# Optimization experiments

Hardware: AMD Instinct MI355X
Metric: run time of the kernel (lower is better)

The kernel has to match this reference:

```python
import jax, jax.numpy as jnp
import numpy as np

N = 65536   # batch_size * timeseries
D = 512     # feature dim of h_real
K = 64      # n_clusters


def setup_inputs() -> dict:
    key = jax.random.key(0)
    k1, k2 = jax.random.split(key)
    h_real = jax.random.normal(k1, (N, D), dtype=jnp.float32)
    # F is an (approximately) orthogonal projection parameter [N, K].
    F = jax.random.normal(k2, (N, K), dtype=jnp.float32)
    return {"h_real": h_real, "F": F}


def reference(h_real, F):
    # Original: WTW = h h^T (N x N); loss = trace(WTW) - trace(F^T WTW F).
    # Algebraically identical reduced form, never materializing the N x N Gram:
    #   trace(h h^T) = sum(h * h)
    #   trace(F^T h h^T F) = ||F^T h||_F^2
    tr_wtw = jnp.sum(h_real * h_real)
    G = F.T @ h_real                      # [K, D] skinny GEMM
    tr_proj = jnp.sum(G * G)
    return tr_wtw - tr_proj
```

## Files before the change

kernel.cpp:

```cpp
#include <hip/hip_runtime.h>
#include <hip/hip_fp16.h>

#define N_TOT 65536
#define D_DIM 512
#define K_DIM 64
#define NC    32
#define HT_S  40
#define GSZ   (K_DIM * D_DIM)

typedef __bf16   bf16x8 __attribute__((ext_vector_type(8)));
typedef float    f32x4  __attribute__((ext_vector_type(4)));
typedef float    f32x2  __attribute__((ext_vector_type(2)));
typedef _Float16 half8  __attribute__((ext_vector_type(8)));

__device__ __forceinline__ unsigned int pack_bf16(float a, float b) {
    union { float f; unsigned int u; } x, y;
    x.f = a; y.f = b;
    unsigned int lo = (x.u + 0x7fffu + ((x.u >> 16) & 1u)) >> 16;
    unsigned int hi = (y.u + 0x7fffu + ((y.u >> 16) & 1u)) >> 16;
    return lo | (hi << 16);
}

extern "C" __global__ void __launch_bounds__(1024)
k1_partial(const float* __restrict__ h, const float* __restrict__ F,
           float* __restrict__ trw_out, unsigned short* __restrict__ gpart,
           float* __restrict__ out, int rowsPerBlock) {
    __shared__ unsigned short ht[2][D_DIM * HT_S];
    __shared__ unsigned short Ft[2][K_DIM * HT_S];
    __shared__ float red[16];

    const int tid = threadIdx.x;
    const int b   = blockIdx.x;
    if (b == 0 && tid == 0) out[0] = 0.0f;

    const int row0    = b * rowsPerBlock;
    const int nChunks = rowsPerBlock / NC;

    const int sd = tid & 127;
    const int sg = tid >> 7;
    const int fk = (tid & 31) * 2;
    const int fg = tid >> 5;
    const int wave = tid >> 6;
    const int lane = tid & 63;
    const int m    = lane & 15;
    const int q    = lane >> 4;

    f32x4 acc[4][2];
    #pragma unroll
    for (int kt = 0; kt < 4; ++kt)
        #pragma unroll
        for (int dt = 0; dt < 2; ++dt)
            acc[kt][dt] = (f32x4){0.f, 0.f, 0.f, 0.f};

    float trw = 0.f;

    auto stage = [&](int c, int p) {
        const int r0 = row0 + c * NC;
        const float* hb = h + (size_t)(r0 + sg * 4) * D_DIM + sd * 4;
        f32x4 v[4];
        #pragma unroll
        for (int j = 0; j < 4; ++j)
            v[j] = *(const f32x4*)(hb + (size_t)j * D_DIM);
        #pragma unroll
        for (int j = 0; j < 4; ++j)
            #pragma unroll
            for (int e = 0; e < 4; ++e)
                trw += v[j][e] * v[j][e];
        #pragma unroll
        for (int e = 0; e < 4; ++e) {
            uint2 pk;
            pk.x = pack_bf16(v[0][e], v[1][e]);
            pk.y = pack_bf16(v[2][e], v[3][e]);
            *(uint2*)&ht[p][(sd * 4 + e) * HT_S + sg * 4] = pk;
        }
        if (tid < 256) {
            const float* fb = F + (size_t)(r0 + fg * 4) * K_DIM + fk;
            f32x2 w[4];
            #pragma unroll
            for (int j = 0; j < 4; ++j)
                w[j] = *(const f32x2*)(fb + (size_t)j * K_DIM);
            #pragma unroll
            for (int e = 0; e < 2; ++e) {
                uint2 pk;
                pk.x = pack_bf16(w[0][e], w[1][e]);
                pk.y = pack_bf16(w[2][e], w[3][e]);
                *(uint2*)&Ft[p][(fk + e) * HT_S + fg * 4] = pk;
            }
        }
    };

    stage(0, 0);

    for (int c = 0; c < nChunks; ++c) {
        __syncthreads();
        if (c + 1 < nChunks) stage(c + 1, (c + 1) & 1);

        const int p = c & 1;
        bf16x8 bfrag[2], afrag[4];
        #pragma unroll
        for (int dt = 0; dt < 2; ++dt)
            bfrag[dt] = *(const bf16x8*)&ht[p][(wave * 32 + dt * 16 + m) * HT_S + q * 8];
        #pragma unroll
        for (int kt = 0; kt < 4; ++kt)
            afrag[kt] = *(const bf16x8*)&Ft[p][(kt * 16 + m) * HT_S + q * 8];
        #pragma unroll
        for (int kt = 0; kt < 4; ++kt)
            #pragma unroll
            for (int dt = 0; dt < 2; ++dt)
                acc[kt][dt] = __builtin_amdgcn_mfma_f32_16x16x32_bf16(
                    afrag[kt], bfrag[dt], acc[kt][dt], 0, 0, 0);
    }

    __syncthreads();
    unsigned short* gt = &ht[0][0];
    #pragma unroll
    for (int kt = 0; kt < 4; ++kt)
        #pragma unroll
        for (int dt = 0; dt < 2; ++dt)
            #pragma unroll
            for (int r = 0; r < 4; ++r) {
                const int k = kt * 16 + q * 4 + r;
                const int d = wave * 32 + dt * 16 + m;
                __half hv = __float2half(acc[kt][dt][r]);
                gt[k * D_DIM + d] = *(unsigned short*)&hv;
            }

    #pragma unroll
    for (int off = 32; off > 0; off >>= 1) trw += __shfl_down(trw, off, 64);
    if (lane == 0) red[wave] = trw;
    __syncthreads();

    unsigned short* gp = gpart + (size_t)b * GSZ;
    #pragma unroll
    for (int it = 0; it < 4; ++it)
        *(uint4*)(gp + it * 8192 + tid * 8) = *(const uint4*)(gt + it * 8192 + tid * 8);

    if (tid == 0) {
        float s = 0.f;
        #pragma unroll
        for (int w = 0; w < 16; ++w) s += red[w];
        trw_out[b] = s;
    }
}

extern "C" __global__ void __launch_bounds__(512)
k2_reduce(const float* __restrict__ trw, const unsigned short* __restrict__ gpart,
          float* __restrict__ out, int P) {
    __shared__ float sh[32 * 16 * 8];
    __shared__ float red2[8];

    const int tid = threadIdx.x;
    const int sub = tid >> 4;
    const int oct = tid & 15;
    const int tt  = blockIdx.x * 16 + oct;

    float g[8];
    #pragma unroll
    for (int j = 0; j < 8; ++j) g[j] = 0.f;

    const unsigned short* base = gpart + (size_t)tt * 8;
    for (int b = sub; b < P; b += 32) {
        half8 v = *(const half8*)(base + (size_t)b * GSZ);
        #pragma unroll
        for (int j = 0; j < 8; ++j) g[j] += (float)v[j];
    }
    #pragma unroll
    for (int j = 0; j < 8; ++j) sh[(sub * 16 + oct) * 8 + j] = g[j];
    __syncthreads();

    float val = 0.f;
    if (tid < 128) {
        const int o2 = tid >> 3, j = tid & 7;
        float s = 0.f;
        #pragma unroll
        for (int sb = 0; sb < 32; ++sb) s += sh[(sb * 16 + o2) * 8 + j];
        val = -s * s;
    } else if (blockIdx.x == 0 && tid - 128 < P) {
        val = trw[tid - 128];
    }

    #pragma unroll
    for (int off = 32; off > 0; off >>= 1) val += __shfl_down(val, off, 64);
    if ((tid & 63) == 0) red2[tid >> 6] = val;
    __syncthreads();
    if (tid == 0) {
        float s = 0.f;
        #pragma unroll
        for (int w = 0; w < 8; ++w) s += red2[w];
        atomicAdd(out, s);
    }
}

extern "C" void kernel_launch(void* const* d_in, const int* in_sizes, int n_in,
                              void* d_out, int out_size, void* d_ws, size_t ws_size,
                              hipStream_t stream) {
    const float* h = (const float*)d_in[0];
    const float* F = (const float*)d_in[1];
    float* out = (float*)d_out;

    int P = 256;
    while (P > 1 && (size_t)4096 + (size_t)P * (GSZ * 2) > ws_size) P >>= 1;
    const int rowsPerBlock = N_TOT / P;

    float* trw = (float*)d_ws;
    unsigned short* gpart = (unsigned short*)((char*)d_ws + 4096);

    hipLaunchKernelGGL(k1_partial, dim3(P), dim3(1024), 0, stream,
                       h, F, trw, gpart, out, rowsPerBlock);
    hipLaunchKernelGGL(k2_reduce, dim3(256), dim3(512), 0, stream,
                       trw, gpart, out, P);
}
```

Measured before the change: 212.3 us.

## Fuse partial GEMM and reduction into one cooperative kernel with register prefetch

Merges the per-block partial GEMM kernel and the cross-block reduction kernel into a single cooperative launch. A grid-wide sync separates the two phases, and each block then reduces its own slice of the fp16 partials. This removes the second kernel launch and its dependency gap. The main loop is also restructured so global loads of h for the next two chunks sit in two register buffers and are issued before the MFMA step, with bf16 packing into LDS afterward, to hide load latency. This raises register pressure, adds grid-sync overhead, and needs every block resident at once; if the cooperative launch fails, the old two-kernel path runs instead.

```diff
diff --git a/kernel.cpp b/kernel.cpp
--- a/kernel.cpp
+++ b/kernel.cpp
@@ -1,5 +1,8 @@
 #include <hip/hip_runtime.h>
 #include <hip/hip_fp16.h>
+#include <hip/hip_cooperative_groups.h>
+
+namespace cg = cooperative_groups;
 
 #define N_TOT 65536
 #define D_DIM 512
@@ -22,12 +25,13 @@
 }
 
 extern "C" __global__ void __launch_bounds__(1024)
-k1_partial(const float* __restrict__ h, const float* __restrict__ F,
-           float* __restrict__ trw_out, unsigned short* __restrict__ gpart,
-           float* __restrict__ out, int rowsPerBlock) {
+fused(const float* __restrict__ h, const float* __restrict__ F,
+      unsigned short* __restrict__ gpart, float* __restrict__ out,
+      int rowsPerBlock, int P) {
     __shared__ unsigned short ht[2][D_DIM * HT_S];
     __shared__ unsigned short Ft[2][K_DIM * HT_S];
     __shared__ float red[16];
+    __shared__ float sTrw;
 
     const int tid = threadIdx.x;
     const int b   = blockIdx.x;
@@ -53,6 +57,196 @@
             acc[kt][dt] = (f32x4){0.f, 0.f, 0.f, 0.f};
 
     float trw = 0.f;
+    f32x4 hA[4], hB[4];
+    f32x2 Fw[4];
+
+    auto issueH = [&](int c, f32x4 (&dst)[4]) {
+        const float* hb = h + (size_t)(row0 + c * NC + sg * 4) * D_DIM + sd * 4;
+        #pragma unroll
+        for (int j = 0; j < 4; ++j)
+            dst[j] = *(const f32x4*)(hb + (size_t)j * D_DIM);
+    };
+    auto issueF = [&](int c) {
+        if (tid < 256) {
+            const float* fb = F + (size_t)(row0 + c * NC + fg * 4) * K_DIM + fk;
+            #pragma unroll
+            for (int j = 0; j < 4; ++j)
+                Fw[j] = *(const f32x2*)(fb + (size_t)j * K_DIM);
+        }
+    };
+    auto packH = [&](f32x4 (&v)[4], int p) {
+        #pragma unroll
+        for (int j = 0; j < 4; ++j)
+            #pragma unroll
+            for (int e = 0; e < 4; ++e)
+                trw += v[j][e] * v[j][e];
+        #pragma unroll
+        for (int e = 0; e < 4; ++e) {
+            uint2 pk;
+            pk.x = pack_bf16(v[0][e], v[1][e]);
+            pk.y = pack_bf16(v[2][e], v[3][e]);
+            *(uint2*)&ht[p][(sd * 4 + e) * HT_S + sg * 4] = pk;
+        }
+    };
+    auto packF = [&](int p) {
+        if (tid < 256) {
+            #pragma unroll
+            for (int e = 0; e < 2; ++e) {
+                uint2 pk;
+                pk.x = pack_bf16(Fw[0][e], Fw[1][e]);
+                pk.y = pack_bf16(Fw[2][e], Fw[3][e]);
+                *(uint2*)&Ft[p][(fk + e) * HT_S + fg * 4] = pk;
+            }
+        }
+    };
+    auto mfmaStep = [&](int c) {
+        const int p = c & 1;
+        bf16x8 bfrag[2], afrag[4];
+        #pragma unroll
+        for (int dt = 0; dt < 2; ++dt)
+            bfrag[dt] = *(const bf16x8*)&ht[p][(wave * 32 + dt * 16 + m) * HT_S + q * 8];
+        #pragma unroll
+        for (int kt = 0; kt < 4; ++kt)
+            afrag[kt] = *(const bf16x8*)&Ft[p][(kt * 16 + m) * HT_S + q * 8];
+        #pragma unroll
+        for (int kt = 0; kt < 4; ++kt)
+            #pragma unroll
+            for (int dt = 0; dt < 2; ++dt)
+                acc[kt][dt] = __builtin_amdgcn_mfma_f32_16x16x32_bf16(
+                    afrag[kt], bfrag[dt], acc[kt][dt], 0, 0, 0);
+    };
+
+    issueH(0, hA);
+    issueH(1, hB);
+    issueF(0);
+    packF(0);
+    packH(hA, 0);
+
+    for (int c = 0; c < nChunks; c += 2) {
+        __syncthreads();
+        if (c + 2 < nChunks) issueH(c + 2, hA);
+        if (c + 1 < nChunks) issueF(c + 1);
+        mfmaStep(c);
+        if (c + 1 < nChunks) { packF((c + 1) & 1); packH(hB, (c + 1) & 1); }
+
+        if (c + 1 < nChunks) {
+            __syncthreads();
+            if (c + 3 < nChunks) issueH(c + 3, hB);
+            if (c + 2 < nChunks) issueF(c + 2);
+            mfmaStep(c + 1);
+            if (c + 2 < nChunks) { packF((c + 2) & 1); packH(hA, (c + 2) & 1); }
+        }
+    }
+
+    __syncthreads();
+    unsigned short* gt = &ht[0][0];
+    #pragma unroll
+    for (int kt = 0; kt < 4; ++kt)
+        #pragma unroll
+        for (int dt = 0; dt < 2; ++dt)
+            #pragma unroll
+            for (int r = 0; r < 4; ++r) {
+                const int k = kt * 16 + q * 4 + r;
+                const int d = wave * 32 + dt * 16 + m;
+                __half hv = __float2half(acc[kt][dt][r]);
+                gt[k * D_DIM + d] = *(unsigned short*)&hv;
+            }
+
+    #pragma unroll
+    for (int off = 32; off > 0; off >>= 1) trw += __shfl_down(trw, off, 64);
+    if (lane == 0) red[wave] = trw;
+    __syncthreads();
+
+    unsigned short* gp = gpart + (size_t)b * GSZ;
+    #pragma unroll
+    for (int it = 0; it < 4; ++it)
+        *(uint4*)(gp + it * 8192 + tid * 8) = *(const uint4*)(gt + it * 8192 + tid * 8);
+
+    if (tid == 0) {
+        float s = 0.f;
+        #pragma unroll
+        for (int w = 0; w < 16; ++w) s += red[w];
+        sTrw = s;
+    }
+
+    __threadfence();
+    cg::this_grid().sync();
+
+    float* sh = (float*)&ht[0][0];
+    const int sub = tid >> 4;
+    const int oct = tid & 15;
+    const int nOct = GSZ / 8;
+    float myVal = 0.f;
+
+    for (int pass = 0; pass < nOct / (P * 16); ++pass) {
+        const int tt = pass * P * 16 + b * 16 + oct;
+        float g[8];
+        #pragma unroll
+        for (int j = 0; j < 8; ++j) g[j] = 0.f;
+        const unsigned short* base = gpart + (size_t)tt * 8;
+        for (int bb = sub; bb < P; bb += 64) {
+            half8 v = *(const half8*)(base + (size_t)bb * GSZ);
+            #pragma unroll
+            for (int j = 0; j < 8; ++j) g[j] += (float)v[j];
+        }
+        __syncthreads();
+        #pragma unroll
+        for (int j = 0; j < 8; ++j) sh[(sub * 16 + oct) * 8 + j] = g[j];
+        __syncthreads();
+        if (tid < 128) {
+            const int o2 = tid >> 3, j = tid & 7;
+            float s = 0.f;
+            #pragma unroll
+            for (int sb = 0; sb < 64; ++sb) s += sh[(sb * 16 + o2) * 8 + j];
+            myVal += -s * s;
+        }
+    }
+    if (tid == 0) myVal += sTrw;
+
+    #pragma unroll
+    for (int off = 32; off > 0; off >>= 1) myVal += __shfl_down(myVal, off, 64);
+    if (lane == 0) red[wave] = myVal;
+    __syncthreads();
+    if (tid == 0) {
+        float s = 0.f;
+        #pragma unroll
+        for (int w = 0; w < 16; ++w) s += red[w];
+        atomicAdd(out, s);
+    }
+}
+
+extern "C" __global__ void __launch_bounds__(1024)
+k1_partial(const float* __restrict__ h, const float* __restrict__ F,
+           float* __restrict__ trw_out, unsigned short* __restrict__ gpart,
+           float* __restrict__ out, int rowsPerBlock) {
+    __shared__ unsigned short ht[2][D_DIM * HT_S];
+    __shared__ unsigned short Ft[2][K_DIM * HT_S];
+    __shared__ float red[16];
+
+    const int tid = threadIdx.x;
+    const int b   = blockIdx.x;
+    if (b == 0 && tid == 0) out[0] = 0.0f;
+
+    const int row0    = b * rowsPerBlock;
+    const int nChunks = rowsPerBlock / NC;
+
+    const int sd = tid & 127;
+    const int sg = tid >> 7;
+    const int fk = (tid & 31) * 2;
+    const int fg = tid >> 5;
+    const int wave = tid >> 6;
+    const int lane = tid & 63;
+    const int m    = lane & 15;
+    const int q    = lane >> 4;
+
+    f32x4 acc[4][2];
+    #pragma unroll
+    for (int kt = 0; kt < 4; ++kt)
+        #pragma unroll
+        for (int dt = 0; dt < 2; ++dt)
+            acc[kt][dt] = (f32x4){0.f, 0.f, 0.f, 0.f};
+
+    float trw = 0.f;
 
     auto stage = [&](int c, int p) {
         const int r0 = row0 + c * NC;
@@ -90,11 +284,9 @@
     };
 
     stage(0, 0);
-
     for (int c = 0; c < nChunks; ++c) {
         __syncthreads();
         if (c + 1 < nChunks) stage(c + 1, (c + 1) & 1);
-
         const int p = c & 1;
         bf16x8 bfrag[2], afrag[4];
         #pragma unroll
@@ -200,13 +392,25 @@
 
     int P = 256;
     while (P > 1 && (size_t)4096 + (size_t)P * (GSZ * 2) > ws_size) P >>= 1;
-    const int rowsPerBlock = N_TOT / P;
+    int rowsPerBlock = N_TOT / P;
 
     float* trw = (float*)d_ws;
     unsigned short* gpart = (unsigned short*)((char*)d_ws + 4096);
 
-    hipLaunchKernelGGL(k1_partial, dim3(P), dim3(1024), 0, stream,
-                       h, F, trw, gpart, out, rowsPerBlock);
-    hipLaunchKernelGGL(k2_reduce, dim3(256), dim3(512), 0, stream,
-                       trw, gpart, out, P);
+    void* args[6];
+    args[0] = (void*)&h;
+    args[1] = (void*)&F;
+    args[2] = (void*)&gpart;
+    args[3] = (void*)&out;
+    args[4] = (void*)&rowsPerBlock;
+    args[5] = (void*)&P;
+
+    hipError_t e = hipLaunchCooperativeKernel((const void*)fused, dim3(P), dim3(1024),
+                                              args, 0, stream);
+    if (e != hipSuccess) {
+        hipLaunchKernelGGL(k1_partial, dim3(P), dim3(1024), 0, stream,
+                           h, F, trw, gpart, out, rowsPerBlock);
+        hipLaunchKernelGGL(k2_reduce, dim3(256), dim3(512), 0, stream,
+                           trw, gpart, out, P);
+    }
 }
```

After: 354.7 us. 67.1% more time.
